# Kernel tuning notes

Hardware: AMD Instinct MI355X
Metric: run time of the kernel (lower is better)

The kernel has to match this reference:

```python
import jax, jax.numpy as jnp
import numpy as np

MARGIN = 0.9
WIN = 3
SIGMA = 1.5    # kornia ssim default gaussian sigma
PAD = (WIN - 1) // 2


def _gauss2d(win, sigma):
    x = np.arange(win, dtype=np.float64) - (win - 1) / 2.0
    g = np.exp(-(x ** 2) / (2.0 * sigma ** 2))
    g = g / g.sum()
    return jnp.asarray(np.outer(g, g), dtype=jnp.float32)

_KERN = _gauss2d(WIN, SIGMA)[None, None]


def _blur(z):
    # kornia filter2d: reflect padding + gaussian window, 'same' output
    zp = jnp.pad(z, ((0, 0), (0, 0), (PAD, PAD), (PAD, PAD)), mode='reflect')
    return jax.lax.conv_general_dilated(zp, _KERN.astype(z.dtype), (1, 1), 'VALID')


def setup_inputs() -> dict:
    key = jax.random.key(0)
    kernels = jax.random.normal(key, (128, 128, 3, 3), dtype=jnp.float32)
    return {"kernels": kernels}


def reference(kernels):
    C_in, C_out, h, w = kernels.shape
    flat = kernels.reshape(C_in * C_out, h, w)

    # pair indices (constants) -- replicate torch flatten/repeat_interleave order exactly
    bi, bj = np.triu_indices(C_out, k=1)          # P_per_ch pairs
    P = bi.shape[0]
    offs = np.arange(C_in) * C_out
    i_idx = (bi[:, None] + offs[None, :]).ravel() # [P, C_in] row-major flatten
    j_idx = (bj[:, None] + offs[None, :]).ravel()
    ch_id = jnp.asarray(np.repeat(np.arange(C_in), P), dtype=jnp.int32)

    # dynamic range (torch uses .item() -> detached)
    rng = jax.lax.stop_gradient(flat.max() - flat.min())
    rng = jnp.where(rng == 0, jnp.asarray(1.0, flat.dtype), rng)
    C1 = (0.01 * rng) ** 2
    C2 = (0.03 * rng) ** 2

    x = flat[i_idx][:, None]  # [P_total,1,h,w]
    y = flat[j_idx][:, None]

    mu1, mu2 = _blur(x), _blur(y)
    mu1_sq, mu2_sq, mu12 = mu1 * mu1, mu2 * mu2, mu1 * mu2
    s1 = _blur(x * x) - mu1_sq
    s2 = _blur(y * y) - mu2_sq
    s12 = _blur(x * y) - mu12
    ssim_map = ((2.0 * mu12 + C1) * (2.0 * s12 + C2)) / (
        (mu1_sq + mu2_sq + C1) * (s1 + s2 + C2))
    ssim_pair = ssim_map.mean(axis=(1, 2, 3))           # [P_total]

    hinge = jax.nn.relu(ssim_pair - MARGIN)
    pos = (hinge > 0).astype(flat.dtype)
    sums = jax.ops.segment_sum(hinge, ch_id, num_segments=C_in)
    counts = jax.ops.segment_sum(pos, ch_id, num_segments=C_in)
    layer_loss = (sums / jnp.maximum(counts, 1.0)).mean()
    return layer_loss  # total / n_layers with a single layer
```

## Files before the change

### kernel.cpp

```cpp
#include <hip/hip_runtime.h>
#include <math.h>

#define CIN   128
#define COUT  128
#define NMAPS (CIN*COUT)
#define PPC   8128
#define MSTR  24

__device__ inline unsigned f2key(float f) {
    unsigned b = __float_as_uint(f);
    return (b & 0x80000000u) ? ~b : (b | 0x80000000u);
}
__device__ inline float key2f(unsigned k) {
    unsigned b = (k & 0x80000000u) ? (k ^ 0x80000000u) : ~k;
    return __uint_as_float(b);
}

__device__ inline void blur3d(const double* X, double* O, double g0, double g1) {
    double h0 = 2.0 * g0;
    double T[9];
#pragma unroll
    for (int c = 0; c < 3; ++c) {
        double x0 = X[c], x1 = X[3 + c], x2 = X[6 + c];
        T[c]     = g1 * x0 + h0 * x1;
        T[3 + c] = g0 * (x0 + x2) + g1 * x1;
        T[6 + c] = h0 * x1 + g1 * x2;
    }
#pragma unroll
    for (int r = 0; r < 3; ++r) {
        double t0 = T[3 * r], t1 = T[3 * r + 1], t2 = T[3 * r + 2];
        O[3 * r]     = g1 * t0 + h0 * t1;
        O[3 * r + 1] = g0 * (t0 + t2) + g1 * t1;
        O[3 * r + 2] = h0 * t1 + g1 * t2;
    }
}

__global__ __launch_bounds__(256) void k_init(unsigned* mmx, float* segsum, float* segcnt) {
    int t = threadIdx.x;
    if (t == 0) { mmx[0] = 0xFFFFFFFFu; mmx[1] = 0u; }
    if (t < 128) segsum[t] = 0.0f;
    else         segcnt[t - 128] = 0.0f;
}

__global__ __launch_bounds__(256) void k_pre(const float* __restrict__ in,
                                             double* __restrict__ pre,
                                             unsigned* __restrict__ mmx,
                                             double g0, double g1) {
    int m = blockIdx.x * 256 + threadIdx.x;
    float lmin = 1e30f, lmax = -1e30f;
    float xf[9];
    double x[9];
#pragma unroll
    for (int k = 0; k < 9; ++k) {
        xf[k] = in[m * 9 + k];
        lmin = fminf(lmin, xf[k]);
        lmax = fmaxf(lmax, xf[k]);
        x[k] = (double)xf[k];
    }
    double mu[9];
    blur3d(x, mu, g0, g1);
    double xx[9];
#pragma unroll
    for (int k = 0; k < 9; ++k) xx[k] = x[k] * x[k];
    double bxx[9];
    blur3d(xx, bxx, g0, g1);

    double* p = pre + (size_t)m * MSTR;
    float*  pf = (float*)p;
#pragma unroll
    for (int k = 0; k < 9; ++k) pf[k] = xf[k];
#pragma unroll
    for (int k = 0; k < 9; ++k) {
        p[6 + k]  = mu[k];
        p[15 + k] = bxx[k] - mu[k] * mu[k];
    }
#pragma unroll
    for (int o = 32; o > 0; o >>= 1) {
        lmin = fminf(lmin, __shfl_down(lmin, o));
        lmax = fmaxf(lmax, __shfl_down(lmax, o));
    }
    if ((threadIdx.x & 63) == 0) {
        atomicMin(&mmx[0], f2key(lmin));
        atomicMax(&mmx[1], f2key(lmax));
    }
}

__global__ __launch_bounds__(256) void k_pairs(const double* __restrict__ pre,
                                               const unsigned* __restrict__ mmx,
                                               float* __restrict__ segsum,
                                               float* __restrict__ segcnt,
                                               double g0, double g1) {
    __shared__ double lds[COUT * MSTR];
    __shared__ float lsum[128], lcnt[128];
    int c = blockIdx.x >> 2;
    int q = blockIdx.x & 3;

    if (threadIdx.x < 128) { lsum[threadIdx.x] = 0.0f; lcnt[threadIdx.x] = 0.0f; }

    const float4* src = reinterpret_cast<const float4*>(pre + (size_t)c * COUT * MSTR);
    float4* dst = reinterpret_cast<float4*>(lds);
    for (int t = threadIdx.x; t < COUT * MSTR / 2; t += 256) dst[t] = src[t];
    __syncthreads();

    double rng = (double)key2f(mmx[1]) - (double)key2f(mmx[0]);
    if (rng == 0.0) rng = 1.0;
    double C1 = (0.01 * rng) * (0.01 * rng);
    double C2 = (0.03 * rng) * (0.03 * rng);

    for (int p = threadIdx.x + 256 * q; p < PPC; p += 1024) {
        int a = (int)((255.0f - sqrtf((float)(65025 - 8 * p))) * 0.5f);
        while ((a + 1) * (255 - (a + 1)) / 2 <= p) ++a;
        while (a * (255 - a) / 2 > p) --a;
        int b = a + 1 + (p - a * (255 - a) / 2);

        const double* Pa = lds + a * MSTR;
        const double* Pb = lds + b * MSTR;
        const float*  xa = (const float*)Pa;
        const float*  xb = (const float*)Pb;

        double z[9];
#pragma unroll
        for (int k = 0; k < 9; ++k) z[k] = (double)xa[k] * (double)xb[k];
        double bz[9];
        blur3d(z, bz, g0, g1);

        double ssum = 0.0;
#pragma unroll
        for (int k = 0; k < 9; ++k) {
            double ma = Pa[6 + k], mb = Pb[6 + k];
            double mu12 = ma * mb;
            double s12  = bz[k] - mu12;
            double num  = (2.0 * mu12 + C1) * (2.0 * s12 + C2);
            double den  = (ma * ma + mb * mb + C1) * (Pa[15 + k] + Pb[15 + k] + C2);
            ssum += num / den;
        }
        double hg = ssum / 9.0 - 0.9;
        if (hg > 0.0) {
            unsigned seg = (unsigned)(p * 128 + c) / 8128u;
            atomicAdd(&lsum[seg], (float)hg);
            atomicAdd(&lcnt[seg], 1.0f);
        }
    }
    __syncthreads();
    if (threadIdx.x < 128) {
        float s = lsum[threadIdx.x], n = lcnt[threadIdx.x];
        if (s != 0.0f || n != 0.0f) {
            atomicAdd(&segsum[threadIdx.x], s);
            atomicAdd(&segcnt[threadIdx.x], n);
        }
    }
}

__global__ __launch_bounds__(128) void k_fin(const float* __restrict__ segsum,
                                             const float* __restrict__ segcnt,
                                             float* __restrict__ out) {
    int t = threadIdx.x;
    double v = (double)segsum[t] / fmax((double)segcnt[t], 1.0);
#pragma unroll
    for (int o = 32; o > 0; o >>= 1) v += __shfl_down(v, o);
    __shared__ double ws2[2];
    if ((t & 63) == 0) ws2[t >> 6] = v;
    __syncthreads();
    if (t == 0) out[0] = (float)((ws2[0] + ws2[1]) * (1.0 / 128.0));
}

extern "C" void kernel_launch(void* const* d_in, const int* in_sizes, int n_in,
                              void* d_out, int out_size, void* d_ws, size_t ws_size,
                              hipStream_t stream) {
    const float* in = (const float*)d_in[0];
    float* out = (float*)d_out;
    char* ws = (char*)d_ws;

    unsigned* mmx = (unsigned*)ws;
    float* segsum = (float*)(ws + 256);
    float* segcnt = (float*)(ws + 768);
    double* pre   = (double*)(ws + 2048);

    double e = exp(-1.0 / 4.5);
    double s = 2.0 * e + 1.0;
    double g0 = e / s;
    double g1 = 1.0 / s;

    k_init <<<1, 256, 0, stream>>>(mmx, segsum, segcnt);
    k_pre  <<<NMAPS / 256, 256, 0, stream>>>(in, pre, mmx, g0, g1);
    k_pairs<<<CIN * 4, 256, 0, stream>>>(pre, mmx, segsum, segcnt, g0, g1);
    k_fin  <<<1, 128, 0, stream>>>(segsum, segcnt, out);
}
```

Baseline: 81.11 us.

## Screen pairs in fp32 and recompute near-threshold pairs in fp64

The pair SSIM is now computed in single precision from fp32 precomputed stats, with the per-pixel divisions replaced by one running fraction. Only pairs whose fp32 SSIM exceeds a slightly lowered threshold are appended to a global list, and a new kernel recomputes those pairs in fp64 for the hinge sums. The init kernel is folded into k_pre, and the min/max reduction moves from global atomics to per-block partials that each pair block reduces itself. This targets the cost of fp64 math on every pair, but adds a list atomic, a fourth launch and extra fp64 stores in k_pre. The fixed 0.003 screening margin is what the exact result relies on.

```diff
diff --git a/kernel.cpp b/kernel.cpp
--- a/kernel.cpp
+++ b/kernel.cpp
@@ -5,15 +5,39 @@
 #define COUT  128
 #define NMAPS (CIN*COUT)
 #define PPC   8128
-#define MSTR  24
-
-__device__ inline unsigned f2key(float f) {
-    unsigned b = __float_as_uint(f);
-    return (b & 0x80000000u) ? ~b : (b | 0x80000000u);
-}
-__device__ inline float key2f(unsigned k) {
-    unsigned b = (k & 0x80000000u) ? (k ^ 0x80000000u) : ~k;
-    return __uint_as_float(b);
+#define F32S  27
+#define F64S  24
+#define LCAP  (1u<<21)
+#define BPC   8
+
+
+__device__ inline void decode_pair(int p, int& a, int& b) {
+    int a0 = (int)((255.0f - sqrtf((float)(65025 - 8 * p))) * 0.5f);
+    if (a0 < 0) a0 = 0;
+    if (a0 > 126) a0 = 126;
+    while ((a0 + 1) * (255 - (a0 + 1)) / 2 <= p) ++a0;
+    while (a0 * (255 - a0) / 2 > p) --a0;
+    a = a0;
+    b = a0 + 1 + (p - a0 * (255 - a0) / 2);
+}
+
+__device__ inline void blur3f(const float* X, float* O, float g0, float g1) {
+    float h0 = 2.0f * g0;
+    float T[9];
+#pragma unroll
+    for (int c = 0; c < 3; ++c) {
+        float x0 = X[c], x1 = X[3 + c], x2 = X[6 + c];
+        T[c]     = g1 * x0 + h0 * x1;
+        T[3 + c] = g0 * (x0 + x2) + g1 * x1;
+        T[6 + c] = h0 * x1 + g1 * x2;
+    }
+#pragma unroll
+    for (int r = 0; r < 3; ++r) {
+        float t0 = T[3 * r], t1 = T[3 * r + 1], t2 = T[3 * r + 2];
+        O[3 * r]     = g1 * t0 + h0 * t1;
+        O[3 * r + 1] = g0 * (t0 + t2) + g1 * t1;
+        O[3 * r + 2] = h0 * t1 + g1 * t2;
+    }
 }
 
 __device__ inline void blur3d(const double* X, double* O, double g0, double g1) {
@@ -35,93 +59,176 @@
     }
 }
 
-__global__ __launch_bounds__(256) void k_init(unsigned* mmx, float* segsum, float* segcnt) {
-    int t = threadIdx.x;
-    if (t == 0) { mmx[0] = 0xFFFFFFFFu; mmx[1] = 0u; }
-    if (t < 128) segsum[t] = 0.0f;
-    else         segcnt[t - 128] = 0.0f;
-}
 
 __global__ __launch_bounds__(256) void k_pre(const float* __restrict__ in,
-                                             double* __restrict__ pre,
-                                             unsigned* __restrict__ mmx,
+                                             float* __restrict__ pre32,
+                                             double* __restrict__ pre64,
+                                             float* __restrict__ pbmin,
+                                             float* __restrict__ pbmax,
+                                             float* __restrict__ segsum,
+                                             float* __restrict__ segcnt,
+                                             unsigned* __restrict__ listc,
+                                             float g0f, float g1f,
                                              double g0, double g1) {
-    int m = blockIdx.x * 256 + threadIdx.x;
+    __shared__ float stg[2304];
+    int tid = threadIdx.x;
+    int base = blockIdx.x * 2304;
+    for (int i = tid; i < 2304; i += 256) stg[i] = in[base + i];
+    __syncthreads();
+
+    float xf[9];
     float lmin = 1e30f, lmax = -1e30f;
-    float xf[9];
-    double x[9];
 #pragma unroll
     for (int k = 0; k < 9; ++k) {
-        xf[k] = in[m * 9 + k];
+        xf[k] = stg[tid * 9 + k];
         lmin = fminf(lmin, xf[k]);
         lmax = fmaxf(lmax, xf[k]);
-        x[k] = (double)xf[k];
-    }
-    double mu[9];
-    blur3d(x, mu, g0, g1);
-    double xx[9];
-#pragma unroll
-    for (int k = 0; k < 9; ++k) xx[k] = x[k] * x[k];
-    double bxx[9];
-    blur3d(xx, bxx, g0, g1);
-
-    double* p = pre + (size_t)m * MSTR;
-    float*  pf = (float*)p;
-#pragma unroll
-    for (int k = 0; k < 9; ++k) pf[k] = xf[k];
-#pragma unroll
-    for (int k = 0; k < 9; ++k) {
-        p[6 + k]  = mu[k];
-        p[15 + k] = bxx[k] - mu[k] * mu[k];
-    }
+    }
+    int m = blockIdx.x * 256 + tid;
+
+    {
+        float mu[9], q[9], bq[9];
+        blur3f(xf, mu, g0f, g1f);
+#pragma unroll
+        for (int k = 0; k < 9; ++k) q[k] = xf[k] * xf[k];
+        blur3f(q, bq, g0f, g1f);
+        float* o = pre32 + m * F32S;
+#pragma unroll
+        for (int k = 0; k < 9; ++k) {
+            o[k]      = xf[k];
+            o[9 + k]  = mu[k];
+            o[18 + k] = bq[k] - mu[k] * mu[k];
+        }
+    }
+    {
+        double xd[9], mud[9], qd[9], bqd[9];
+#pragma unroll
+        for (int k = 0; k < 9; ++k) xd[k] = (double)xf[k];
+        blur3d(xd, mud, g0, g1);
+#pragma unroll
+        for (int k = 0; k < 9; ++k) qd[k] = xd[k] * xd[k];
+        blur3d(qd, bqd, g0, g1);
+        double* od = pre64 + (size_t)m * F64S;
+        float* odf = (float*)od;
+#pragma unroll
+        for (int k = 0; k < 9; ++k) odf[k] = xf[k];
+#pragma unroll
+        for (int k = 0; k < 9; ++k) {
+            od[6 + k]  = mud[k];
+            od[15 + k] = bqd[k] - mud[k] * mud[k];
+        }
+    }
+
 #pragma unroll
     for (int o = 32; o > 0; o >>= 1) {
         lmin = fminf(lmin, __shfl_down(lmin, o));
         lmax = fmaxf(lmax, __shfl_down(lmax, o));
     }
-    if ((threadIdx.x & 63) == 0) {
-        atomicMin(&mmx[0], f2key(lmin));
-        atomicMax(&mmx[1], f2key(lmax));
-    }
-}
-
-__global__ __launch_bounds__(256) void k_pairs(const double* __restrict__ pre,
-                                               const unsigned* __restrict__ mmx,
-                                               float* __restrict__ segsum,
-                                               float* __restrict__ segcnt,
-                                               double g0, double g1) {
-    __shared__ double lds[COUT * MSTR];
-    __shared__ float lsum[128], lcnt[128];
-    int c = blockIdx.x >> 2;
-    int q = blockIdx.x & 3;
-
-    if (threadIdx.x < 128) { lsum[threadIdx.x] = 0.0f; lcnt[threadIdx.x] = 0.0f; }
-
-    const float4* src = reinterpret_cast<const float4*>(pre + (size_t)c * COUT * MSTR);
-    float4* dst = reinterpret_cast<float4*>(lds);
-    for (int t = threadIdx.x; t < COUT * MSTR / 2; t += 256) dst[t] = src[t];
-    __syncthreads();
-
-    double rng = (double)key2f(mmx[1]) - (double)key2f(mmx[0]);
-    if (rng == 0.0) rng = 1.0;
-    double C1 = (0.01 * rng) * (0.01 * rng);
-    double C2 = (0.03 * rng) * (0.03 * rng);
-
-    for (int p = threadIdx.x + 256 * q; p < PPC; p += 1024) {
-        int a = (int)((255.0f - sqrtf((float)(65025 - 8 * p))) * 0.5f);
-        while ((a + 1) * (255 - (a + 1)) / 2 <= p) ++a;
-        while (a * (255 - a) / 2 > p) --a;
-        int b = a + 1 + (p - a * (255 - a) / 2);
-
-        const double* Pa = lds + a * MSTR;
-        const double* Pb = lds + b * MSTR;
-        const float*  xa = (const float*)Pa;
-        const float*  xb = (const float*)Pb;
-
-        double z[9];
+    __shared__ float rmn[4], rmx[4];
+    if ((tid & 63) == 0) { rmn[tid >> 6] = lmin; rmx[tid >> 6] = lmax; }
+    __syncthreads();
+    if (tid == 0) {
+        pbmin[blockIdx.x] = fminf(fminf(rmn[0], rmn[1]), fminf(rmn[2], rmn[3]));
+        pbmax[blockIdx.x] = fmaxf(fmaxf(rmx[0], rmx[1]), fmaxf(rmx[2], rmx[3]));
+    }
+    if (blockIdx.x == 0) {
+        if (tid < 128) { segsum[tid] = 0.0f; segcnt[tid] = 0.0f; }
+        if (tid == 128) *listc = 0u;
+    }
+}
+
+
+__global__ __launch_bounds__(256) void k_pairs(const float* __restrict__ pre32,
+                                               const float* __restrict__ pbmin,
+                                               const float* __restrict__ pbmax,
+                                               unsigned* __restrict__ listc,
+                                               unsigned* __restrict__ list,
+                                               double* __restrict__ c12,
+                                               float g0f, float g1f) {
+    __shared__ float P[COUT * F32S];
+    __shared__ float cc[2];
+    int tid = threadIdx.x;
+    int c = blockIdx.x >> 3, q = blockIdx.x & 7;
+
+    const float* src = pre32 + (size_t)c * COUT * F32S;
+    for (int i = tid; i < COUT * F32S; i += 256) P[i] = src[i];
+
+    if (tid < 64) {
+        float mn = pbmin[tid], mx = pbmax[tid];
+#pragma unroll
+        for (int o = 32; o > 0; o >>= 1) {
+            mn = fminf(mn, __shfl_down(mn, o));
+            mx = fmaxf(mx, __shfl_down(mx, o));
+        }
+        if (tid == 0) {
+            double rng = (double)mx - (double)mn;
+            if (rng == 0.0) rng = 1.0;
+            double C1 = (0.01 * rng) * (0.01 * rng);
+            double C2 = (0.03 * rng) * (0.03 * rng);
+            cc[0] = (float)C1; cc[1] = (float)C2;
+            if (blockIdx.x == 0) { c12[0] = C1; c12[1] = C2; }
+        }
+    }
+    __syncthreads();
+    float C1 = cc[0], C2 = cc[1];
+
+#pragma unroll
+    for (int it = 0; it < 4; ++it) {
+        int p = it * 2048 + q * 256 + tid;
+        if (p >= PPC) break;
+        int a, b;
+        decode_pair(p, a, b);
+        const float* A = P + a * F32S;
+        const float* B = P + b * F32S;
+
+        float z[9], bz[9];
+#pragma unroll
+        for (int k = 0; k < 9; ++k) z[k] = A[k] * B[k];
+        blur3f(z, bz, g0f, g1f);
+
+        float an = 0.0f, ad = 1.0f;
+#pragma unroll
+        for (int k = 0; k < 9; ++k) {
+            float ma = A[9 + k], mb = B[9 + k];
+            float mu12 = ma * mb;
+            float s12  = bz[k] - mu12;
+            float nn = fmaf(2.0f, mu12, C1) * fmaf(2.0f, s12, C2);
+            float dd = fmaf(ma, ma, fmaf(mb, mb, C1)) * (A[18 + k] + B[18 + k] + C2);
+            an = an * dd + nn * ad;
+            ad *= dd;
+        }
+        float ssim = an / (ad * 9.0f);
+        if (ssim > 0.897f) {
+            unsigned idx = atomicAdd(listc, 1u);
+            if (idx < LCAP) list[idx] = (unsigned)((c << 13) | p);
+        }
+    }
+}
+
+
+__global__ __launch_bounds__(256) void k_fb(const double* __restrict__ pre64,
+                                            const unsigned* __restrict__ listc,
+                                            const unsigned* __restrict__ list,
+                                            const double* __restrict__ c12,
+                                            float* __restrict__ segsum,
+                                            float* __restrict__ segcnt,
+                                            double g0, double g1) {
+    unsigned n = *listc;
+    if (n > LCAP) n = LCAP;
+    double C1 = c12[0], C2 = c12[1];
+    for (unsigned i = blockIdx.x * 256 + threadIdx.x; i < n; i += gridDim.x * 256) {
+        unsigned u = list[i];
+        int c = (int)(u >> 13), p = (int)(u & 8191);
+        int a, b;
+        decode_pair(p, a, b);
+        const double* Pa = pre64 + ((size_t)c * COUT + a) * F64S;
+        const double* Pb = pre64 + ((size_t)c * COUT + b) * F64S;
+        const float* xa = (const float*)Pa;
+        const float* xb = (const float*)Pb;
+
+        double z[9], bz[9];
 #pragma unroll
         for (int k = 0; k < 9; ++k) z[k] = (double)xa[k] * (double)xb[k];
-        double bz[9];
         blur3d(z, bz, g0, g1);
 
         double ssum = 0.0;
@@ -137,19 +244,12 @@
         double hg = ssum / 9.0 - 0.9;
         if (hg > 0.0) {
             unsigned seg = (unsigned)(p * 128 + c) / 8128u;
-            atomicAdd(&lsum[seg], (float)hg);
-            atomicAdd(&lcnt[seg], 1.0f);
-        }
-    }
-    __syncthreads();
-    if (threadIdx.x < 128) {
-        float s = lsum[threadIdx.x], n = lcnt[threadIdx.x];
-        if (s != 0.0f || n != 0.0f) {
-            atomicAdd(&segsum[threadIdx.x], s);
-            atomicAdd(&segcnt[threadIdx.x], n);
-        }
-    }
-}
+            atomicAdd(&segsum[seg], (float)hg);
+            atomicAdd(&segcnt[seg], 1.0f);
+        }
+    }
+}
+
 
 __global__ __launch_bounds__(128) void k_fin(const float* __restrict__ segsum,
                                              const float* __restrict__ segcnt,
@@ -163,6 +263,7 @@
     __syncthreads();
     if (t == 0) out[0] = (float)((ws2[0] + ws2[1]) * (1.0 / 128.0));
 }
+
 
 extern "C" void kernel_launch(void* const* d_in, const int* in_sizes, int n_in,
                               void* d_out, int out_size, void* d_ws, size_t ws_size,
@@ -171,18 +272,24 @@
     float* out = (float*)d_out;
     char* ws = (char*)d_ws;
 
-    unsigned* mmx = (unsigned*)ws;
-    float* segsum = (float*)(ws + 256);
-    float* segcnt = (float*)(ws + 768);
-    double* pre   = (double*)(ws + 2048);
+    float*    pbmin  = (float*)(ws + 0);
+    float*    pbmax  = (float*)(ws + 256);
+    float*    segsum = (float*)(ws + 512);
+    float*    segcnt = (float*)(ws + 1024);
+    unsigned* listc  = (unsigned*)(ws + 1536);
+    double*   c12    = (double*)(ws + 1544);
+    float*    pre32  = (float*)(ws + 2048);
+    double*   pre64  = (double*)(ws + 2048 + 1769472);
+    unsigned* list   = (unsigned*)(ws + 2048 + 1769472 + 3145728);
 
     double e = exp(-1.0 / 4.5);
     double s = 2.0 * e + 1.0;
-    double g0 = e / s;
-    double g1 = 1.0 / s;
-
-    k_init <<<1, 256, 0, stream>>>(mmx, segsum, segcnt);
-    k_pre  <<<NMAPS / 256, 256, 0, stream>>>(in, pre, mmx, g0, g1);
-    k_pairs<<<CIN * 4, 256, 0, stream>>>(pre, mmx, segsum, segcnt, g0, g1);
+    double g0 = e / s, g1 = 1.0 / s;
+    float g0f = (float)g0, g1f = (float)g1;
+
+    k_pre  <<<NMAPS / 256, 256, 0, stream>>>(in, pre32, pre64, pbmin, pbmax,
+                                             segsum, segcnt, listc, g0f, g1f, g0, g1);
+    k_pairs<<<CIN * BPC, 256, 0, stream>>>(pre32, pbmin, pbmax, listc, list, c12, g0f, g1f);
+    k_fb   <<<128, 256, 0, stream>>>(pre64, listc, list, c12, segsum, segcnt, g0, g1);
     k_fin  <<<1, 128, 0, stream>>>(segsum, segcnt, out);
 }
```

New measurement: 78.79 us. 2.9% less time.
